# Kernel optimization log

Measured on AMD Instinct MI355X. Metric: run time of the kernel, lower is better.

The kernel has to match this reference:

```python
import jax, jax.numpy as jnp
import numpy as np

EPS = 1e-5
SLOPE = 0.2

def _leaky(x):
    return jnp.where(x >= 0, x, SLOPE * x)

def _bn(x, g, b, axes):
    # batch-norm in training mode: biased stats over `axes`, per remaining channel dim
    mu = jnp.mean(x, axis=axes, keepdims=True)
    var = jnp.var(x, axis=axes, keepdims=True)
    shape = [1] * x.ndim
    shape[2 if x.ndim == 5 else 1] = -1
    return (x - mu) * jax.lax.rsqrt(var + EPS) * g.reshape(shape) + b.reshape(shape)

def setup_inputs() -> dict:
    key = jax.random.key(0)
    ks = jax.random.split(key, 6)
    T, B, C, H, W, D = 17, 16, 512, 16, 16, 256
    return {
        "cond": jax.random.normal(ks[0], (B, D), jnp.float32),
        "xbar": jax.random.normal(ks[1], (T, B, C, H, W), jnp.float32),
        "lin_w": jax.random.normal(ks[2], (D, D), jnp.float32) * 0.05,
        "lin_b": jnp.zeros((D,), jnp.float32),
        "bn_s_g": jnp.ones((D,), jnp.float32),
        "bn_s_b": jnp.zeros((D,), jnp.float32),
        "conv1_w": jax.random.normal(ks[3], (C, C), jnp.float32) * 0.05,
        "bn1_g": jnp.ones((C,), jnp.float32),
        "bn1_b": jnp.zeros((C,), jnp.float32),
        "conv2_w": jax.random.normal(ks[4], (C, C + D), jnp.float32) * 0.05,
        "bn2_g": jnp.ones((C,), jnp.float32),
        "bn2_b": jnp.zeros((C,), jnp.float32),
        "conv3_w": jax.random.normal(ks[5], (1, C, 2, 2), jnp.float32) * 0.05,
    }

def reference(cond, xbar, lin_w, lin_b, bn_s_g, bn_s_b, conv1_w, bn1_g, bn1_b, conv2_w, bn2_g, bn2_b, conv3_w):
    # sent_map: Linear -> BatchNorm1d (over batch) -> LeakyReLU
    sent = cond @ lin_w.T + lin_b                       # [B, D]
    sent = _leaky(_bn(sent, bn_s_g, bn_s_b, axes=(0,)))

    motions = xbar[1:] - xbar[:-1]                      # [F, B, C, H, W]
    F, B, C, H, W = motions.shape

    # motion_map: 1x1 conv -> BN (per-frame stats, matching the python loop) -> LeakyReLU
    h = jnp.einsum('fbchw,oc->fbohw', motions, conv1_w)
    h = _leaky(_bn(h, bn1_g, bn1_b, axes=(1, 3, 4)))

    # broadcast sentence vector over space (replaces per-pixel python loop)
    sent_dupe = jnp.broadcast_to(sent[None, :, :, None, None], (F, B, sent.shape[1], H, W))
    ms = jnp.concatenate([h, sent_dupe], axis=2)        # [F, B, C+D, H, W]

    # predictor: 1x1 conv -> BN (per-frame) -> LeakyReLU -> 2x2 stride-2 conv
    h2 = jnp.einsum('fbchw,oc->fbohw', ms, conv2_w)
    h2 = _leaky(_bn(h2, bn2_g, bn2_b, axes=(1, 3, 4)))

    h2f = h2.reshape(F * B, C, H, W)
    out = jax.lax.conv_general_dilated(
        h2f, conv3_w, window_strides=(2, 2), padding='VALID',
        dimension_numbers=('NCHW', 'OIHW', 'NCHW'))     # [F*B, 1, H/2, W/2]
    return out.reshape(F, B, -1)                        # matches view(B,-1) per frame + stack
```

## Files before the change

### kernel.cpp

```cpp
#include <hip/hip_runtime.h>
#include <hip/hip_bf16.h>

#define EPS 1e-5f
#define SLOPE 0.2f

#define NF 16
#define NBATCH 16
#define NC 512
#define NHW 256
#define ND 256
#define K2 768
#define MF 4096
#define FRAME_ELEMS ((size_t)MF * NC)

typedef __attribute__((ext_vector_type(8))) short short8;
typedef __attribute__((ext_vector_type(4))) float float4v;

__device__ __forceinline__ float lrelu(float v) { return v >= 0.f ? v : SLOPE * v; }
__device__ __forceinline__ float b2f(ushort u) { union { float f; uint i; } x; x.i = ((uint)u) << 16; return x.f; }
__device__ __forceinline__ ushort f2b(float f) {
  uint i = __float_as_uint(f);
  return (ushort)((i + 0x7FFFu + ((i >> 16) & 1u)) >> 16);
}
__device__ __forceinline__ void gl16(const void* g, void* l) {
  __builtin_amdgcn_global_load_lds(
      (const __attribute__((address_space(1))) unsigned int*)g,
      (__attribute__((address_space(3))) unsigned int*)l, 16, 0, 0);
}
#define SB __builtin_amdgcn_sched_barrier(0)

__global__ __launch_bounds__(256) void k_pre(
    const float* __restrict__ w1, const float* __restrict__ w2,
    const float* __restrict__ cond, const float* __restrict__ lin_w,
    const float* __restrict__ lin_b, const float* __restrict__ gam,
    const float* __restrict__ bet,
    ushort* __restrict__ w1b, ushort* __restrict__ w2b,
    float* __restrict__ bias2) {
  int bx = blockIdx.x, t = threadIdx.x;
  if (bx < 1024) {
    int i = bx * 256 + t;
    w1b[i] = f2b(w1[i]);
    int o = i >> 9, c = i & 511;
    w2b[i] = f2b(w2[(size_t)o * K2 + c]);
    return;
  }
  __shared__ float sl[NBATCH][ND];
  int d = t;
  {
    float acc[NBATCH];
    float bias = lin_b[d];
#pragma unroll
    for (int b = 0; b < NBATCH; ++b) acc[b] = bias;
    for (int k = 0; k < ND; ++k) {
      float w = lin_w[d * ND + k];
#pragma unroll
      for (int b = 0; b < NBATCH; ++b) acc[b] = fmaf(cond[b * ND + k], w, acc[b]);
    }
    float mu = 0.f;
#pragma unroll
    for (int b = 0; b < NBATCH; ++b) mu += acc[b];
    mu *= (1.f / NBATCH);
    float var = 0.f;
#pragma unroll
    for (int b = 0; b < NBATCH; ++b) { float x = acc[b] - mu; var = fmaf(x, x, var); }
    var *= (1.f / NBATCH);
    float sc = rsqrtf(var + EPS) * gam[d];
    float sh = bet[d] - mu * sc;
#pragma unroll
    for (int b = 0; b < NBATCH; ++b) sl[b][d] = lrelu(fmaf(acc[b], sc, sh));
  }
  __syncthreads();
  int o = (bx - 1024) * 256 + t;
  float acc2[NBATCH];
#pragma unroll
  for (int b = 0; b < NBATCH; ++b) acc2[b] = 0.f;
  for (int d2 = 0; d2 < ND; ++d2) {
    float wv = w2[(size_t)o * K2 + NC + d2];
#pragma unroll
    for (int b = 0; b < NBATCH; ++b) acc2[b] = fmaf(sl[b][d2], wv, acc2[b]);
  }
#pragma unroll
  for (int b = 0; b < NBATCH; ++b) bias2[b * NC + o] = acc2[b];
}

__global__ __launch_bounds__(256) void k_mot(
    const float* __restrict__ xbar, ushort* __restrict__ mot, int f0, int nb) {
  __shared__ ushort T2[64][72];
  int t = threadIdx.x;
  int b = blockIdx.y;
  int hw0 = (blockIdx.x & 3) * 64;
  int c0 = (blockIdx.x >> 2) * 64;
  int fg = blockIdx.z * 4;
  int fe = fg + 4 < nb ? fg + 4 : nb;

  int c4 = t >> 4;
  int h16 = t & 15;
  const size_t fstride = (size_t)NBATCH * NC * NHW;
  const float* base = xbar + ((size_t)(f0 + fg) * NBATCH + b) * (NC * NHW) +
                      (size_t)(c0 + c4 * 4) * NHW + hw0 + h16 * 4;

  float4 prev[4], cur[4], nxt[4];
#pragma unroll
  for (int r = 0; r < 4; ++r) prev[r] = *(const float4*)(base + (size_t)r * NHW);
#pragma unroll
  for (int r = 0; r < 4; ++r) cur[r] = *(const float4*)(base + fstride + (size_t)r * NHW);

  for (int fr = fg; fr < fe; ++fr) {
    if (fr + 1 < fe) {
      const float* xn = base + (size_t)(fr - fg + 2) * fstride;
#pragma unroll
      for (int r = 0; r < 4; ++r) nxt[r] = *(const float4*)(xn + (size_t)r * NHW);
    }
#pragma unroll
    for (int i = 0; i < 4; ++i) {
      ushort4 pk = make_ushort4(
          f2b(((const float*)&cur[0])[i] - ((const float*)&prev[0])[i]),
          f2b(((const float*)&cur[1])[i] - ((const float*)&prev[1])[i]),
          f2b(((const float*)&cur[2])[i] - ((const float*)&prev[2])[i]),
          f2b(((const float*)&cur[3])[i] - ((const float*)&prev[3])[i]));
      *(ushort4*)&T2[h16 * 4 + i][c4 * 4] = pk;
    }
    __syncthreads();
    ushort* mp = mot + ((size_t)fr * MF + b * NHW + hw0) * NC + c0;
#pragma unroll
    for (int it = 0; it < 2; ++it) {
      int unit = it * 256 + t;
      int hw = unit >> 3, q = unit & 7;
      short8 v = *(const short8*)&T2[hw][q * 8];
      *(short8*)&mp[(size_t)hw * NC + q * 8] = v;
    }
    __syncthreads();
#pragma unroll
    for (int r = 0; r < 4; ++r) { prev[r] = cur[r]; cur[r] = nxt[r]; }
  }
}

template <int BIAS>
__global__ __launch_bounds__(512, 2) void k_gemm8(
    const ushort* __restrict__ A, const ushort* __restrict__ W,
    const float* __restrict__ bias2, ushort* __restrict__ H,
    float2* __restrict__ part) {
  __shared__ ushort lds[65536];
  const int t = threadIdx.x, w = t >> 6, l = t & 63;
  const int g = blockIdx.z, bx = blockIdx.x, ny = blockIdx.y;
  const int m0 = bx * 256, n0 = ny * 256;
  const int wr = w >> 2, wc = w & 3;

  const ushort* Ag = A + (size_t)g * FRAME_ELEMS + (size_t)m0 * NC;
  const ushort* Wg = W + (size_t)n0 * NC;

  size_t goff[4];
  int loff[4];
#pragma unroll
  for (int q = 0; q < 4; ++q) {
    int u = w * 256 + q * 64 + l;
    int row = u >> 3, cb = (u & 7) ^ (row & 7);
    goff[q] = (size_t)row * NC + cb * 8;
    loff[q] = u * 8;
  }

#define STAGE8(t_, b_)                                               \
  do {                                                               \
    const int k0_ = (t_) * 64;                                       \
    _Pragma("unroll") for (int q = 0; q < 4; ++q)                    \
        gl16(Ag + goff[q] + k0_, &lds[(b_) * 32768 + loff[q]]);      \
    _Pragma("unroll") for (int q = 0; q < 4; ++q)                    \
        gl16(Wg + goff[q] + k0_, &lds[(b_) * 32768 + 16384 + loff[q]]); \
  } while (0)

  int slot[2];
#pragma unroll
  for (int kk = 0; kk < 2; ++kk) slot[kk] = (((kk * 4 + (l >> 4)) ^ (l & 7)) * 8);

  float4v acc[8][4];
#pragma unroll
  for (int i = 0; i < 8; ++i)
#pragma unroll
    for (int j = 0; j < 4; ++j) acc[i][j] = (float4v)0.f;

  STAGE8(0, 0);
  STAGE8(1, 1);
  asm volatile("s_waitcnt vmcnt(8)" ::: "memory"); SB;
  __builtin_amdgcn_s_barrier(); SB;

#pragma unroll
  for (int kt = 0; kt < 8; ++kt) {
    const int b = kt & 1;
    const ushort* la = &lds[b * 32768];
    const ushort* lb = la + 16384;
    short8 bf[4][2], af[4][2];
#pragma unroll
    for (int fn = 0; fn < 4; ++fn) {
      int r = wc * 64 + fn * 16 + (l & 15);
#pragma unroll
      for (int kk = 0; kk < 2; ++kk)
        bf[fn][kk] = *(const short8*)&lb[r * 64 + slot[kk]];
    }
#pragma unroll
    for (int fm = 0; fm < 4; ++fm) {
      int r = wr * 128 + fm * 16 + (l & 15);
#pragma unroll
      for (int kk = 0; kk < 2; ++kk)
        af[fm][kk] = *(const short8*)&la[r * 64 + slot[kk]];
    }
    asm volatile("s_waitcnt lgkmcnt(0)" ::: "memory"); SB;
    __builtin_amdgcn_s_setprio(1);
#pragma unroll
    for (int kk = 0; kk < 2; ++kk)
#pragma unroll
      for (int fm = 0; fm < 4; ++fm)
#pragma unroll
        for (int fn = 0; fn < 4; ++fn)
          acc[fm][fn] = __builtin_amdgcn_mfma_f32_16x16x32_bf16(
              af[fm][kk], bf[fn][kk], acc[fm][fn], 0, 0, 0);
    __builtin_amdgcn_s_setprio(0);
#pragma unroll
    for (int fm = 0; fm < 4; ++fm) {
      int r = wr * 128 + 64 + fm * 16 + (l & 15);
#pragma unroll
      for (int kk = 0; kk < 2; ++kk)
        af[fm][kk] = *(const short8*)&la[r * 64 + slot[kk]];
    }
    asm volatile("s_waitcnt lgkmcnt(0)" ::: "memory"); SB;
    __builtin_amdgcn_s_barrier(); SB;
    if (kt < 6) STAGE8(kt + 2, b);
    __builtin_amdgcn_s_setprio(1);
#pragma unroll
    for (int kk = 0; kk < 2; ++kk)
#pragma unroll
      for (int fm = 0; fm < 4; ++fm)
#pragma unroll
        for (int fn = 0; fn < 4; ++fn)
          acc[fm + 4][fn] = __builtin_amdgcn_mfma_f32_16x16x32_bf16(
              af[fm][kk], bf[fn][kk], acc[fm + 4][fn], 0, 0, 0);
    __builtin_amdgcn_s_setprio(0);
    if (kt < 7) {
      if (kt < 6) asm volatile("s_waitcnt vmcnt(8)" ::: "memory");
      else        asm volatile("s_waitcnt vmcnt(0)" ::: "memory");
      SB;
      __builtin_amdgcn_s_barrier(); SB;
    }
  }
#undef STAGE8

  SB; __builtin_amdgcn_s_barrier(); SB;

  float bz[4];
#pragma unroll
  for (int fn = 0; fn < 4; ++fn)
    bz[fn] = BIAS ? bias2[bx * NC + n0 + wc * 64 + fn * 16 + (l & 15)] : 0.f;

  float sv[4], qv[4];
#pragma unroll
  for (int fn = 0; fn < 4; ++fn) {
    float s = 0.f, q = 0.f;
#pragma unroll
    for (int fm = 0; fm < 8; ++fm)
#pragma unroll
      for (int j = 0; j < 4; ++j) {
        float v = acc[fm][fn][j] + bz[fn];
        acc[fm][fn][j] = v;
        s += v;
        q = fmaf(v, v, q);
      }
    s += __shfl_xor(s, 16); s += __shfl_xor(s, 32);
    q += __shfl_xor(q, 16); q += __shfl_xor(q, 32);
    sv[fn] = s; qv[fn] = q;
  }
  if (l < 16) {
    int mb = bx * 2 + wr;
    float2* pp = part + ((size_t)g * 32 + mb) * NC + n0 + wc * 64 + l;
#pragma unroll
    for (int fn = 0; fn < 4; ++fn) pp[fn * 16] = make_float2(sv[fn], qv[fn]);
  }

  ushort* ep = &lds[w * 1088];
  ushort* Hg = H + ((size_t)g * MF + m0 + wr * 128) * NC + n0 + wc * 64;
#pragma unroll
  for (int fm = 0; fm < 8; ++fm) {
#pragma unroll
    for (int fn = 0; fn < 4; ++fn)
#pragma unroll
      for (int j = 0; j < 4; ++j)
        ep[((l >> 4) * 4 + j) * 68 + fn * 16 + (l & 15)] = f2b(acc[fm][fn][j]);
#pragma unroll
    for (int h = 0; h < 2; ++h) {
      int r = h * 8 + (l >> 3), sl = l & 7;
      short8 v = *(const short8*)&ep[r * 68 + sl * 8];
      *(short8*)&Hg[(size_t)(fm * 16 + r) * NC + sl * 8] = v;
    }
  }
}

__global__ __launch_bounds__(256) void k_stats2(
    const float2* __restrict__ part, const float* __restrict__ gam,
    const float* __restrict__ bet, float2* __restrict__ st) {
  int bi = blockIdx.x;
  int g = bi >> 1;
  int o = (bi & 1) * 256 + threadIdx.x;
  float s = 0.f, q = 0.f;
#pragma unroll
  for (int mb = 0; mb < 32; ++mb) {
    float2 v = part[((size_t)g * 32 + mb) * NC + o];
    s += v.x;
    q += v.y;
  }
  float mu = s * (1.f / 4096.f);
  float var = q * (1.f / 4096.f) - mu * mu;
  float sc = rsqrtf(var + EPS) * gam[o];
  st[g * NC + o] = make_float2(sc, bet[o] - mu * sc);
}

__global__ __launch_bounds__(256) void k_act(
    const ushort* __restrict__ h1, const float2* __restrict__ st,
    ushort* __restrict__ a1) {
  int g = blockIdx.z;
  size_t i0 = ((size_t)blockIdx.x * 256 + threadIdx.x) * 8;
  int o0 = (int)(i0 & 511);
  const ushort* src = h1 + (size_t)g * FRAME_ELEMS + i0;
  ushort* dst = a1 + (size_t)g * FRAME_ELEMS + i0;
  short8 v = *(const short8*)src;
  short8 r;
#pragma unroll
  for (int e = 0; e < 8; ++e) {
    float2 ss = st[g * NC + o0 + e];
    float x = fmaf(b2f((ushort)v[e]), ss.x, ss.y);
    r[e] = (short)f2b(lrelu(x));
  }
  *(short8*)dst = r;
}

__global__ __launch_bounds__(256) void k_conv3(
    const ushort* __restrict__ h2, const float2* __restrict__ st2,
    const float* __restrict__ w3, float* __restrict__ out, int f0) {
  int g = blockIdx.z;
  int b = blockIdx.x >> 2;
  int q = blockIdx.x & 3;
  int t = threadIdx.x;
  int oi = q * 16 + (t >> 4);
  int cs = t & 15;
  int y = oi >> 3, x = oi & 7;
  const ushort* base = h2 + ((size_t)g * MF + b * NHW) * NC;
  int m00 = (2 * y) * 16 + 2 * x;
  float acc = 0.f;
#pragma unroll
  for (int c8 = cs * 32; c8 < cs * 32 + 32; c8 += 8) {
    short8 v0 = *(const short8*)&base[(size_t)(m00 + 0) * NC + c8];
    short8 v1 = *(const short8*)&base[(size_t)(m00 + 1) * NC + c8];
    short8 v2 = *(const short8*)&base[(size_t)(m00 + 16) * NC + c8];
    short8 v3 = *(const short8*)&base[(size_t)(m00 + 17) * NC + c8];
#pragma unroll
    for (int e = 0; e < 8; ++e) {
      float2 ss = st2[g * NC + c8 + e];
      float4 wv = ((const float4*)w3)[c8 + e];
      acc = fmaf(lrelu(fmaf(b2f((ushort)v0[e]), ss.x, ss.y)), wv.x, acc);
      acc = fmaf(lrelu(fmaf(b2f((ushort)v1[e]), ss.x, ss.y)), wv.y, acc);
      acc = fmaf(lrelu(fmaf(b2f((ushort)v2[e]), ss.x, ss.y)), wv.z, acc);
      acc = fmaf(lrelu(fmaf(b2f((ushort)v3[e]), ss.x, ss.y)), wv.w, acc);
    }
  }
  acc += __shfl_xor(acc, 1);
  acc += __shfl_xor(acc, 2);
  acc += __shfl_xor(acc, 4);
  acc += __shfl_xor(acc, 8);
  if (cs == 0) out[((size_t)(f0 + g) * NBATCH + b) * 64 + oi] = acc;
}

extern "C" void kernel_launch(void* const* d_in, const int* in_sizes, int n_in,
                              void* d_out, int out_size, void* d_ws, size_t ws_size,
                              hipStream_t stream) {
  const float* cond = (const float*)d_in[0];
  const float* xbar = (const float*)d_in[1];
  const float* lin_w = (const float*)d_in[2];
  const float* lin_b = (const float*)d_in[3];
  const float* bnsg = (const float*)d_in[4];
  const float* bnsb = (const float*)d_in[5];
  const float* w1 = (const float*)d_in[6];
  const float* bn1g = (const float*)d_in[7];
  const float* bn1b = (const float*)d_in[8];
  const float* w2 = (const float*)d_in[9];
  const float* bn2g = (const float*)d_in[10];
  const float* bn2b = (const float*)d_in[11];
  const float* w3 = (const float*)d_in[12];
  float* out = (float*)d_out;

  char* p = (char*)d_ws;
  float* bias2 = (float*)p;   p += ((NBATCH * NC * 4 + 255) & ~255);
  float2* st1 = (float2*)p;   p += ((NF * NC * 8 + 255) & ~255);
  float2* st2 = (float2*)p;   p += ((NF * NC * 8 + 255) & ~255);
  float2* part = (float2*)p;  p += (((size_t)NF * 32 * NC * 8 + 255) & ~255);
  ushort* w1b = (ushort*)p;   p += ((NC * NC * 2 + 255) & ~255);
  ushort* w2b = (ushort*)p;   p += ((NC * NC * 2 + 255) & ~255);
  size_t used = (size_t)(p - (char*)d_ws);
  const size_t frame_bytes = FRAME_ELEMS * 2;
  size_t rem = ws_size > used ? ws_size - used : 0;
  int FB = (int)(rem / (3 * frame_bytes));
  if (FB < 1) FB = 1;
  if (FB > NF) FB = NF;
  ushort* bufA = (ushort*)p;
  ushort* bufB = bufA + (size_t)FB * FRAME_ELEMS;
  ushort* bufC = bufB + (size_t)FB * FRAME_ELEMS;

  k_pre<<<1026, 256, 0, stream>>>(w1, w2, cond, lin_w, lin_b, bnsg, bnsb,
                                  w1b, w2b, bias2);

  for (int f0 = 0; f0 < NF; f0 += FB) {
    int nb = (NF - f0) < FB ? (NF - f0) : FB;
    int ngrp = (nb + 3) / 4;
    k_mot<<<dim3(32, NBATCH, ngrp), 256, 0, stream>>>(xbar, bufA, f0, nb);
    k_gemm8<0><<<dim3(16, 2, nb), 512, 0, stream>>>(bufA, w1b, nullptr, bufB, part);
    k_stats2<<<2 * nb, 256, 0, stream>>>(part, bn1g, bn1b, st1);
    k_act<<<dim3(1024, 1, nb), 256, 0, stream>>>(bufB, st1, bufA);
    k_gemm8<1><<<dim3(16, 2, nb), 512, 0, stream>>>(bufA, w2b, bias2, bufC, part);
    k_stats2<<<2 * nb, 256, 0, stream>>>(part, bn2g, bn2b, st2);
    k_conv3<<<dim3(NBATCH * 4, 1, nb), 256, 0, stream>>>(bufC, st2, w3, out, f0);
  }
}
```

Baseline: 255.2 us.

## Switch GEMM inner loop to 32x32x16 bf16 MFMA with retiled fragments

Replaces the 16x16x32 MFMA tiles in the pointwise-conv GEMM with 32x32x16 bf16 MFMAs. Each wave now covers its 128x64 output with a 4x2 grid of 32x32 accumulators, and the LDS fragment addressing, swizzle slots, stats reduction and bf16 epilogue transpose are redone for the new accumulator layout. The goal is fewer MFMA issues and fewer LDS fragment reads per unit of compute. Launch bounds drop from 2 to 1 block per SM, which frees registers but may lower occupancy and latency hiding.

```diff
diff --git a/kernel.cpp b/kernel.cpp
--- a/kernel.cpp
+++ b/kernel.cpp
@@ -15,6 +15,7 @@
 
 typedef __attribute__((ext_vector_type(8))) short short8;
 typedef __attribute__((ext_vector_type(4))) float float4v;
+typedef __attribute__((ext_vector_type(16))) float float16v;
 
 __device__ __forceinline__ float lrelu(float v) { return v >= 0.f ? v : SLOPE * v; }
 __device__ __forceinline__ float b2f(ushort u) { union { float f; uint i; } x; x.i = ((uint)u) << 16; return x.f; }
@@ -136,7 +137,7 @@
 }
 
 template <int BIAS>
-__global__ __launch_bounds__(512, 2) void k_gemm8(
+__global__ __launch_bounds__(512, 1) void k_gemm8(
     const ushort* __restrict__ A, const ushort* __restrict__ W,
     const float* __restrict__ bias2, ushort* __restrict__ H,
     float2* __restrict__ part) {
@@ -168,15 +169,21 @@
         gl16(Wg + goff[q] + k0_, &lds[(b_) * 32768 + 16384 + loff[q]]); \
   } while (0)
 
-  int slot[2];
-#pragma unroll
-  for (int kk = 0; kk < 2; ++kk) slot[kk] = (((kk * 4 + (l >> 4)) ^ (l & 7)) * 8);
-
-  float4v acc[8][4];
-#pragma unroll
-  for (int i = 0; i < 8; ++i)
-#pragma unroll
-    for (int j = 0; j < 4; ++j) acc[i][j] = (float4v)0.f;
+  int slot[4];
+#pragma unroll
+  for (int ks = 0; ks < 4; ++ks) slot[ks] = (((ks * 2 + (l >> 5)) ^ (l & 7)) * 8);
+
+  int arow[4], brow[2];
+#pragma unroll
+  for (int fm = 0; fm < 4; ++fm) arow[fm] = (wr * 128 + fm * 32 + (l & 31)) * 64;
+#pragma unroll
+  for (int fn = 0; fn < 2; ++fn) brow[fn] = 16384 + (wc * 64 + fn * 32 + (l & 31)) * 64;
+
+  float16v acc[4][2];
+#pragma unroll
+  for (int i = 0; i < 4; ++i)
+#pragma unroll
+    for (int j = 0; j < 2; ++j) acc[i][j] = (float16v)0.f;
 
   STAGE8(0, 0);
   STAGE8(1, 1);
@@ -186,53 +193,51 @@
 #pragma unroll
   for (int kt = 0; kt < 8; ++kt) {
     const int b = kt & 1;
-    const ushort* la = &lds[b * 32768];
-    const ushort* lb = la + 16384;
-    short8 bf[4][2], af[4][2];
-#pragma unroll
-    for (int fn = 0; fn < 4; ++fn) {
-      int r = wc * 64 + fn * 16 + (l & 15);
-#pragma unroll
-      for (int kk = 0; kk < 2; ++kk)
-        bf[fn][kk] = *(const short8*)&lb[r * 64 + slot[kk]];
-    }
-#pragma unroll
-    for (int fm = 0; fm < 4; ++fm) {
-      int r = wr * 128 + fm * 16 + (l & 15);
-#pragma unroll
-      for (int kk = 0; kk < 2; ++kk)
-        af[fm][kk] = *(const short8*)&la[r * 64 + slot[kk]];
-    }
+    const ushort* lb = &lds[b * 32768];
+    short8 bf[2][2], af[4][2];
+#pragma unroll
+    for (int fn = 0; fn < 2; ++fn)
+#pragma unroll
+      for (int ks = 0; ks < 2; ++ks)
+        bf[fn][ks] = *(const short8*)&lb[brow[fn] + slot[ks]];
+#pragma unroll
+    for (int fm = 0; fm < 4; ++fm)
+#pragma unroll
+      for (int ks = 0; ks < 2; ++ks)
+        af[fm][ks] = *(const short8*)&lb[arow[fm] + slot[ks]];
     asm volatile("s_waitcnt lgkmcnt(0)" ::: "memory"); SB;
     __builtin_amdgcn_s_setprio(1);
 #pragma unroll
-    for (int kk = 0; kk < 2; ++kk)
+    for (int ks = 0; ks < 2; ++ks)
 #pragma unroll
       for (int fm = 0; fm < 4; ++fm)
 #pragma unroll
-        for (int fn = 0; fn < 4; ++fn)
-          acc[fm][fn] = __builtin_amdgcn_mfma_f32_16x16x32_bf16(
-              af[fm][kk], bf[fn][kk], acc[fm][fn], 0, 0, 0);
+        for (int fn = 0; fn < 2; ++fn)
+          acc[fm][fn] = __builtin_amdgcn_mfma_f32_32x32x16_bf16(
+              af[fm][ks], bf[fn][ks], acc[fm][fn], 0, 0, 0);
     __builtin_amdgcn_s_setprio(0);
 #pragma unroll
-    for (int fm = 0; fm < 4; ++fm) {
-      int r = wr * 128 + 64 + fm * 16 + (l & 15);
-#pragma unroll
-      for (int kk = 0; kk < 2; ++kk)
-        af[fm][kk] = *(const short8*)&la[r * 64 + slot[kk]];
-    }
+    for (int fn = 0; fn < 2; ++fn)
+#pragma unroll
+      for (int ks = 0; ks < 2; ++ks)
+        bf[fn][ks] = *(const short8*)&lb[brow[fn] + slot[2 + ks]];
+#pragma unroll
+    for (int fm = 0; fm < 4; ++fm)
+#pragma unroll
+      for (int ks = 0; ks < 2; ++ks)
+        af[fm][ks] = *(const short8*)&lb[arow[fm] + slot[2 + ks]];
     asm volatile("s_waitcnt lgkmcnt(0)" ::: "memory"); SB;
     __builtin_amdgcn_s_barrier(); SB;
     if (kt < 6) STAGE8(kt + 2, b);
     __builtin_amdgcn_s_setprio(1);
 #pragma unroll
-    for (int kk = 0; kk < 2; ++kk)
+    for (int ks = 0; ks < 2; ++ks)
 #pragma unroll
       for (int fm = 0; fm < 4; ++fm)
 #pragma unroll
-        for (int fn = 0; fn < 4; ++fn)
-          acc[fm + 4][fn] = __builtin_amdgcn_mfma_f32_16x16x32_bf16(
-              af[fm][kk], bf[fn][kk], acc[fm + 4][fn], 0, 0, 0);
+        for (int fn = 0; fn < 2; ++fn)
+          acc[fm][fn] = __builtin_amdgcn_mfma_f32_32x32x16_bf16(
+              af[fm][ks], bf[fn][ks], acc[fm][fn], 0, 0, 0);
     __builtin_amdgcn_s_setprio(0);
     if (kt < 7) {
       if (kt < 6) asm volatile("s_waitcnt vmcnt(8)" ::: "memory");
@@ -245,49 +250,49 @@
 
   SB; __builtin_amdgcn_s_barrier(); SB;
 
-  float bz[4];
-#pragma unroll
-  for (int fn = 0; fn < 4; ++fn)
-    bz[fn] = BIAS ? bias2[bx * NC + n0 + wc * 64 + fn * 16 + (l & 15)] : 0.f;
-
-  float sv[4], qv[4];
-#pragma unroll
-  for (int fn = 0; fn < 4; ++fn) {
+  float bz[2];
+#pragma unroll
+  for (int fn = 0; fn < 2; ++fn)
+    bz[fn] = BIAS ? bias2[bx * NC + n0 + wc * 64 + fn * 32 + (l & 31)] : 0.f;
+
+#pragma unroll
+  for (int fn = 0; fn < 2; ++fn) {
     float s = 0.f, q = 0.f;
 #pragma unroll
-    for (int fm = 0; fm < 8; ++fm)
-#pragma unroll
-      for (int j = 0; j < 4; ++j) {
-        float v = acc[fm][fn][j] + bz[fn];
-        acc[fm][fn][j] = v;
+    for (int fm = 0; fm < 4; ++fm)
+#pragma unroll
+      for (int reg = 0; reg < 16; ++reg) {
+        float v = acc[fm][fn][reg] + bz[fn];
+        acc[fm][fn][reg] = v;
         s += v;
         q = fmaf(v, v, q);
       }
-    s += __shfl_xor(s, 16); s += __shfl_xor(s, 32);
-    q += __shfl_xor(q, 16); q += __shfl_xor(q, 32);
-    sv[fn] = s; qv[fn] = q;
-  }
-  if (l < 16) {
-    int mb = bx * 2 + wr;
-    float2* pp = part + ((size_t)g * 32 + mb) * NC + n0 + wc * 64 + l;
-#pragma unroll
-    for (int fn = 0; fn < 4; ++fn) pp[fn * 16] = make_float2(sv[fn], qv[fn]);
-  }
-
-  ushort* ep = &lds[w * 1088];
+    s += __shfl_xor(s, 32);
+    q += __shfl_xor(q, 32);
+    if (l < 32) {
+      int mb = bx * 2 + wr;
+      part[((size_t)g * 32 + mb) * NC + n0 + wc * 64 + fn * 32 + l] =
+          make_float2(s, q);
+    }
+  }
+
+  ushort* ep = &lds[w * 2432];
   ushort* Hg = H + ((size_t)g * MF + m0 + wr * 128) * NC + n0 + wc * 64;
 #pragma unroll
-  for (int fm = 0; fm < 8; ++fm) {
-#pragma unroll
-    for (int fn = 0; fn < 4; ++fn)
-#pragma unroll
-      for (int j = 0; j < 4; ++j)
-        ep[((l >> 4) * 4 + j) * 68 + fn * 16 + (l & 15)] = f2b(acc[fm][fn][j]);
-#pragma unroll
-    for (int h = 0; h < 2; ++h) {
-      int r = h * 8 + (l >> 3), sl = l & 7;
-      short8 v = *(const short8*)&ep[r * 68 + sl * 8];
-      *(short8*)&Hg[(size_t)(fm * 16 + r) * NC + sl * 8] = v;
+  for (int fm = 0; fm < 4; ++fm) {
+#pragma unroll
+    for (int fn = 0; fn < 2; ++fn)
+#pragma unroll
+      for (int reg = 0; reg < 16; ++reg) {
+        int r32 = (reg & 3) + 8 * (reg >> 2) + 4 * (l >> 5);
+        ep[r32 * 76 + fn * 32 + (l & 31)] = f2b(acc[fm][fn][reg]);
+      }
+#pragma unroll
+    for (int it = 0; it < 4; ++it) {
+      int u = it * 64 + l;
+      int r = u >> 3, q = u & 7;
+      short8 v = *(const short8*)&ep[r * 76 + q * 8];
+      *(short8*)&Hg[(size_t)(fm * 32 + r) * NC + q * 8] = v;
     }
   }
 }
```

Measured after the change: 262.3 us. 1.03x slower.
